# Kernel tuning notes

Hardware: AMD Instinct MI355X
Metric: run time of the kernel (lower is better)

## Reference

```python
import jax, jax.numpy as jnp
import numpy as np

N = 16384
E = 524288
D_IN, D_HID, D_OUT = 3, 16, 16


def setup_inputs() -> dict:
    key = jax.random.key(0)
    ks = jax.random.split(key, 8)
    node_feats = jax.random.normal(ks[0], (N, D_IN), dtype=jnp.float32)
    edge_idx = jax.random.randint(ks[1], (2, E), 0, N, dtype=jnp.int64)
    # GIN MLP params (Linear(3,16) -> ReLU -> Linear(16,16) -> ReLU), train_eps
    s1 = 1.0 / np.sqrt(D_IN)
    s2 = 1.0 / np.sqrt(D_HID)
    W1 = jax.random.uniform(ks[2], (D_IN, D_HID), jnp.float32, -s1, s1)
    b1 = jax.random.uniform(ks[3], (D_HID,), jnp.float32, -s1, s1)
    W2 = jax.random.uniform(ks[4], (D_HID, D_OUT), jnp.float32, -s2, s2)
    b2 = jax.random.uniform(ks[5], (D_OUT,), jnp.float32, -s2, s2)
    eps = jnp.zeros((), dtype=jnp.float32)  # PyG init eps=0, trainable
    return {"node_feats": node_feats, "edge_idx": edge_idx,
            "W1": W1, "b1": b1, "W2": W2, "b2": b2, "eps": eps}


def reference(node_feats, edge_idx, W1, b1, W2, b2, eps):
    src, tgt = edge_idx[0], edge_idx[1]
    # GIN aggregation: sum of neighbor features via scatter-add over edges
    agg = jax.ops.segment_sum(node_feats[src], tgt, num_segments=N)  # [N, D_IN]
    z = (1.0 + eps) * node_feats + agg
    # 2-layer MLP with ReLU after each linear
    h = jax.nn.relu(z @ W1 + b1)
    h = jax.nn.relu(h @ W2 + b2)  # [N, D_OUT]
    # dense pairwise similarity
    edge_feats = h @ h.T  # [N, N]
    return edge_feats
```

## Files before the change

kernel.cpp:

```cpp
#include <hip/hip_runtime.h>

#define N_NODES 16384
#define N_EDGES 524288
#define TILE_I 16
#define TILE_J 2048

typedef float f32x4 __attribute__((ext_vector_type(4)));

__global__ void scatter_kernel(const int* __restrict__ eidx,
                               const float* __restrict__ x,
                               float* __restrict__ agg) {
    int e = blockIdx.x * blockDim.x + threadIdx.x;
    if (e >= N_EDGES) return;
    int s = eidx[e];
    int t = eidx[N_EDGES + e];
    float f0 = x[s * 3 + 0];
    float f1 = x[s * 3 + 1];
    float f2 = x[s * 3 + 2];
    atomicAdd(&agg[t * 3 + 0], f0);
    atomicAdd(&agg[t * 3 + 1], f1);
    atomicAdd(&agg[t * 3 + 2], f2);
}

__global__ void mlp_kernel(const float* __restrict__ x,
                           const float* __restrict__ agg,
                           const float* __restrict__ W1,
                           const float* __restrict__ b1,
                           const float* __restrict__ W2,
                           const float* __restrict__ b2,
                           const float* __restrict__ eps_p,
                           float* __restrict__ h) {
    int n = blockIdx.x * blockDim.x + threadIdx.x;
    if (n >= N_NODES) return;
    float se = 1.0f + eps_p[0];
    float z0 = se * x[n * 3 + 0] + agg[n * 3 + 0];
    float z1 = se * x[n * 3 + 1] + agg[n * 3 + 1];
    float z2 = se * x[n * 3 + 2] + agg[n * 3 + 2];
    float h1[16];
#pragma unroll
    for (int j = 0; j < 16; ++j) {
        float a = b1[j];
        a += z0 * W1[0 * 16 + j];
        a += z1 * W1[1 * 16 + j];
        a += z2 * W1[2 * 16 + j];
        h1[j] = fmaxf(a, 0.0f);
    }
    float4* h4 = (float4*)&h[n * 16];
#pragma unroll
    for (int oq = 0; oq < 4; ++oq) {
        float4 o;
        float* op = (float*)&o;
#pragma unroll
        for (int c = 0; c < 4; ++c) {
            int oo = oq * 4 + c;
            float a = b2[oo];
#pragma unroll
            for (int j = 0; j < 16; ++j) a += h1[j] * W2[j * 16 + oo];
            op[c] = fmaxf(a, 0.0f);
        }
        h4[oq] = o;
    }
}

__global__ __launch_bounds__(512) void pairwise_kernel(const float* __restrict__ h,
                                                       float* __restrict__ out) {
    __shared__ float hi[TILE_I * 16];
    const int i0 = (blockIdx.x >> 3) * TILE_I;
    const int j0 = (blockIdx.x & 7) * TILE_J;
    const int tid = threadIdx.x;
    const int wid = tid >> 6;
    const int lane = tid & 63;

    if (tid < TILE_I * 4) {
        ((f32x4*)hi)[tid] = ((const f32x4*)h)[(size_t)i0 * 4 + tid];
    }

    const int jbase = j0 + wid * 256 + lane * 4;
    const f32x4* hg = (const f32x4*)h;
    f32x4 hj[16];
#pragma unroll
    for (int jj = 0; jj < 4; ++jj) {
        const size_t jb4 = (size_t)(jbase + jj) * 4;
        f32x4 q0 = hg[jb4 + 0];
        f32x4 q1 = hg[jb4 + 1];
        f32x4 q2 = hg[jb4 + 2];
        f32x4 q3 = hg[jb4 + 3];
        hj[0][jj]  = q0.x;  hj[1][jj]  = q0.y;  hj[2][jj]  = q0.z;  hj[3][jj]  = q0.w;
        hj[4][jj]  = q1.x;  hj[5][jj]  = q1.y;  hj[6][jj]  = q1.z;  hj[7][jj]  = q1.w;
        hj[8][jj]  = q2.x;  hj[9][jj]  = q2.y;  hj[10][jj] = q2.z;  hj[11][jj] = q2.w;
        hj[12][jj] = q3.x;  hj[13][jj] = q3.y;  hj[14][jj] = q3.z;  hj[15][jj] = q3.w;
    }
    __syncthreads();

    f32x4* out4 = (f32x4*)out;
    const size_t obase = (size_t)i0 * (N_NODES / 4) + (size_t)(jbase >> 2);

#pragma unroll
    for (int r = 0; r < TILE_I; ++r) {
        const f32x4* hr = (const f32x4*)&hi[r * 16];
        f32x4 a0 = hr[0], a1 = hr[1], a2 = hr[2], a3 = hr[3];
        f32x4 acc = a0.x * hj[0];
        acc += a0.y * hj[1];
        acc += a0.z * hj[2];
        acc += a0.w * hj[3];
        acc += a1.x * hj[4];
        acc += a1.y * hj[5];
        acc += a1.z * hj[6];
        acc += a1.w * hj[7];
        acc += a2.x * hj[8];
        acc += a2.y * hj[9];
        acc += a2.z * hj[10];
        acc += a2.w * hj[11];
        acc += a3.x * hj[12];
        acc += a3.y * hj[13];
        acc += a3.z * hj[14];
        acc += a3.w * hj[15];
        __builtin_nontemporal_store(acc, &out4[obase + (size_t)r * (N_NODES / 4)]);
    }
}

extern "C" void kernel_launch(void* const* d_in, const int* in_sizes, int n_in,
                              void* d_out, int out_size, void* d_ws, size_t ws_size,
                              hipStream_t stream) {
    const float* node_feats = (const float*)d_in[0];
    const int*   edge_idx   = (const int*)d_in[1];
    const float* W1         = (const float*)d_in[2];
    const float* b1         = (const float*)d_in[3];
    const float* W2         = (const float*)d_in[4];
    const float* b2         = (const float*)d_in[5];
    const float* eps        = (const float*)d_in[6];
    float* out = (float*)d_out;

    float* agg = (float*)d_ws;
    float* h   = (float*)((char*)d_ws + 262144);

    hipMemsetAsync(agg, 0, N_NODES * 3 * sizeof(float), stream);
    scatter_kernel<<<N_EDGES / 256, 256, 0, stream>>>(edge_idx, node_feats, agg);
    mlp_kernel<<<N_NODES / 256, 256, 0, stream>>>(node_feats, agg, W1, b1, W2, b2, eps, h);

    pairwise_kernel<<<8192, 512, 0, stream>>>(h, out);
}
```

Measured before the change: 269.0 us.

## Split scatter atomics across 8 partial buffers and double pairwise row tile

```diff
diff --git a/kernel.cpp b/kernel.cpp
--- a/kernel.cpp
+++ b/kernel.cpp
@@ -2,16 +2,19 @@
 
 #define N_NODES 16384
 #define N_EDGES 524288
-#define TILE_I 16
+#define TILE_I 32
 #define TILE_J 2048
+#define N3 (N_NODES * 3)
 
 typedef float f32x4 __attribute__((ext_vector_type(4)));
 
 __global__ void scatter_kernel(const int* __restrict__ eidx,
                                const float* __restrict__ x,
-                               float* __restrict__ agg) {
+                               float* __restrict__ splits,
+                               int nc_mask) {
     int e = blockIdx.x * blockDim.x + threadIdx.x;
     if (e >= N_EDGES) return;
+    float* agg = splits + (size_t)(blockIdx.x & nc_mask) * N3;
     int s = eidx[e];
     int t = eidx[N_EDGES + e];
     float f0 = x[s * 3 + 0];
@@ -23,7 +26,8 @@
 }
 
 __global__ void mlp_kernel(const float* __restrict__ x,
-                           const float* __restrict__ agg,
+                           const float* __restrict__ splits,
+                           int nc,
                            const float* __restrict__ W1,
                            const float* __restrict__ b1,
                            const float* __restrict__ W2,
@@ -32,10 +36,17 @@
                            float* __restrict__ h) {
     int n = blockIdx.x * blockDim.x + threadIdx.x;
     if (n >= N_NODES) return;
+    float a0 = 0.f, a1 = 0.f, a2 = 0.f;
+    for (int k = 0; k < nc; ++k) {
+        const float* ag = splits + (size_t)k * N3;
+        a0 += ag[n * 3 + 0];
+        a1 += ag[n * 3 + 1];
+        a2 += ag[n * 3 + 2];
+    }
     float se = 1.0f + eps_p[0];
-    float z0 = se * x[n * 3 + 0] + agg[n * 3 + 0];
-    float z1 = se * x[n * 3 + 1] + agg[n * 3 + 1];
-    float z2 = se * x[n * 3 + 2] + agg[n * 3 + 2];
+    float z0 = se * x[n * 3 + 0] + a0;
+    float z1 = se * x[n * 3 + 1] + a1;
+    float z2 = se * x[n * 3 + 2] + a2;
     float h1[16];
 #pragma unroll
     for (int j = 0; j < 16; ++j) {
@@ -131,12 +142,15 @@
     const float* eps        = (const float*)d_in[6];
     float* out = (float*)d_out;
 
-    float* agg = (float*)d_ws;
-    float* h   = (float*)((char*)d_ws + 262144);
+    float* h      = (float*)d_ws;
+    float* splits = (float*)((char*)d_ws + (size_t)N_NODES * 16 * sizeof(float));
 
-    hipMemsetAsync(agg, 0, N_NODES * 3 * sizeof(float), stream);
-    scatter_kernel<<<N_EDGES / 256, 256, 0, stream>>>(edge_idx, node_feats, agg);
-    mlp_kernel<<<N_NODES / 256, 256, 0, stream>>>(node_feats, agg, W1, b1, W2, b2, eps, h);
+    const size_t need8 = (size_t)N_NODES * 16 * 4 + 8 * (size_t)N3 * 4;
+    const int nc = (ws_size >= need8) ? 8 : 1;
 
-    pairwise_kernel<<<8192, 512, 0, stream>>>(h, out);
+    hipMemsetAsync(splits, 0, (size_t)nc * N3 * sizeof(float), stream);
+    scatter_kernel<<<N_EDGES / 256, 256, 0, stream>>>(edge_idx, node_feats, splits, nc - 1);
+    mlp_kernel<<<N_NODES / 256, 256, 0, stream>>>(node_feats, splits, nc, W1, b1, W2, b2, eps, h);
+
+    pairwise_kernel<<<4096, 512, 0, stream>>>(h, out);
 }
```

Result: slower. 310.1 us (+15.3%).

## Fuse edge aggregation and MLP into one per-node-block kernel using shared atomics

Applied to the files above, without the earlier changes.

```diff
diff --git a/kernel.cpp b/kernel.cpp
--- a/kernel.cpp
+++ b/kernel.cpp
@@ -4,61 +4,80 @@
 #define N_EDGES 524288
 #define TILE_I 16
 #define TILE_J 2048
+#define NPB 64
 
 typedef float f32x4 __attribute__((ext_vector_type(4)));
 
-__global__ void scatter_kernel(const int* __restrict__ eidx,
-                               const float* __restrict__ x,
-                               float* __restrict__ agg) {
-    int e = blockIdx.x * blockDim.x + threadIdx.x;
-    if (e >= N_EDGES) return;
-    int s = eidx[e];
-    int t = eidx[N_EDGES + e];
-    float f0 = x[s * 3 + 0];
-    float f1 = x[s * 3 + 1];
-    float f2 = x[s * 3 + 2];
-    atomicAdd(&agg[t * 3 + 0], f0);
-    atomicAdd(&agg[t * 3 + 1], f1);
-    atomicAdd(&agg[t * 3 + 2], f2);
-}
+__global__ __launch_bounds__(512) void agg_mlp_kernel(const int* __restrict__ eidx,
+                                                      const float* __restrict__ x,
+                                                      const float* __restrict__ W1,
+                                                      const float* __restrict__ b1,
+                                                      const float* __restrict__ W2,
+                                                      const float* __restrict__ b2,
+                                                      const float* __restrict__ eps_p,
+                                                      float* __restrict__ h) {
+    __shared__ float lagg[NPB * 3];
+    const int lo = blockIdx.x * NPB;
+    const int tid = threadIdx.x;
 
-__global__ void mlp_kernel(const float* __restrict__ x,
-                           const float* __restrict__ agg,
-                           const float* __restrict__ W1,
-                           const float* __restrict__ b1,
-                           const float* __restrict__ W2,
-                           const float* __restrict__ b2,
-                           const float* __restrict__ eps_p,
-                           float* __restrict__ h) {
-    int n = blockIdx.x * blockDim.x + threadIdx.x;
-    if (n >= N_NODES) return;
-    float se = 1.0f + eps_p[0];
-    float z0 = se * x[n * 3 + 0] + agg[n * 3 + 0];
-    float z1 = se * x[n * 3 + 1] + agg[n * 3 + 1];
-    float z2 = se * x[n * 3 + 2] + agg[n * 3 + 2];
-    float h1[16];
+    if (tid < NPB * 3) lagg[tid] = 0.0f;
+    __syncthreads();
+
+    const int4* tgt4 = (const int4*)(eidx + N_EDGES);
+    const int*  srcs = eidx;
+    const int nq = N_EDGES / 4;
+
+    for (int idx = tid; idx < nq; idx += 512) {
+        const int4 t4 = tgt4[idx];
+        const int e0 = idx * 4;
+#define PROC(tv, ee)                                                     \
+        {                                                                \
+            unsigned d = (unsigned)((tv) - lo);                          \
+            if (d < NPB) {                                               \
+                int s = srcs[ee];                                        \
+                atomicAdd(&lagg[d * 3 + 0], x[(size_t)s * 3 + 0]);       \
+                atomicAdd(&lagg[d * 3 + 1], x[(size_t)s * 3 + 1]);       \
+                atomicAdd(&lagg[d * 3 + 2], x[(size_t)s * 3 + 2]);       \
+            }                                                            \
+        }
+        PROC(t4.x, e0 + 0)
+        PROC(t4.y, e0 + 1)
+        PROC(t4.z, e0 + 2)
+        PROC(t4.w, e0 + 3)
+#undef PROC
+    }
+    __syncthreads();
+
+    if (tid < NPB) {
+        const int n = lo + tid;
+        const float se = 1.0f + eps_p[0];
+        float z0 = se * x[n * 3 + 0] + lagg[tid * 3 + 0];
+        float z1 = se * x[n * 3 + 1] + lagg[tid * 3 + 1];
+        float z2 = se * x[n * 3 + 2] + lagg[tid * 3 + 2];
+        float h1[16];
 #pragma unroll
-    for (int j = 0; j < 16; ++j) {
-        float a = b1[j];
-        a += z0 * W1[0 * 16 + j];
-        a += z1 * W1[1 * 16 + j];
-        a += z2 * W1[2 * 16 + j];
-        h1[j] = fmaxf(a, 0.0f);
-    }
-    float4* h4 = (float4*)&h[n * 16];
+        for (int j = 0; j < 16; ++j) {
+            float a = b1[j];
+            a += z0 * W1[0 * 16 + j];
+            a += z1 * W1[1 * 16 + j];
+            a += z2 * W1[2 * 16 + j];
+            h1[j] = fmaxf(a, 0.0f);
+        }
+        float4* h4 = (float4*)&h[(size_t)n * 16];
 #pragma unroll
-    for (int oq = 0; oq < 4; ++oq) {
-        float4 o;
-        float* op = (float*)&o;
+        for (int oq = 0; oq < 4; ++oq) {
+            float4 o;
+            float* op = (float*)&o;
 #pragma unroll
-        for (int c = 0; c < 4; ++c) {
-            int oo = oq * 4 + c;
-            float a = b2[oo];
+            for (int c = 0; c < 4; ++c) {
+                int oo = oq * 4 + c;
+                float a = b2[oo];
 #pragma unroll
-            for (int j = 0; j < 16; ++j) a += h1[j] * W2[j * 16 + oo];
-            op[c] = fmaxf(a, 0.0f);
+                for (int j = 0; j < 16; ++j) a += h1[j] * W2[j * 16 + oo];
+                op[c] = fmaxf(a, 0.0f);
+            }
+            h4[oq] = o;
         }
-        h4[oq] = o;
     }
 }
 
@@ -131,12 +150,9 @@
     const float* eps        = (const float*)d_in[6];
     float* out = (float*)d_out;
 
-    float* agg = (float*)d_ws;
-    float* h   = (float*)((char*)d_ws + 262144);
+    float* h = (float*)d_ws;
 
-    hipMemsetAsync(agg, 0, N_NODES * 3 * sizeof(float), stream);
-    scatter_kernel<<<N_EDGES / 256, 256, 0, stream>>>(edge_idx, node_feats, agg);
-    mlp_kernel<<<N_NODES / 256, 256, 0, stream>>>(node_feats, agg, W1, b1, W2, b2, eps, h);
-
+    agg_mlp_kernel<<<N_NODES / NPB, 512, 0, stream>>>(edge_idx, node_feats,
+                                                      W1, b1, W2, b2, eps, h);
     pairwise_kernel<<<8192, 512, 0, stream>>>(h, out);
 }
```

Result: slower. 323.4 us (+20.2%).
